# Performance work log

Measured on AMD Instinct MI355X. Metric: run time of the kernel, lower is better.

## Reference

```python
import jax, jax.numpy as jnp
import numpy as np

C = 256
CQK = C // 8


def setup_inputs() -> dict:
    key = jax.random.key(0)
    ks = jax.random.split(key, 8)
    B, H, W = 4, 64, 64
    x = jax.random.normal(ks[0], (B, C, H, W), dtype=jnp.float32)
    # 1x1 conv weights are plain [out_c, in_c] matrices + bias
    sq = 1.0 / np.sqrt(C)
    Wq = jax.random.uniform(ks[1], (CQK, C), jnp.float32, -sq, sq)
    bq = jax.random.uniform(ks[2], (CQK,), jnp.float32, -sq, sq)
    Wk = jax.random.uniform(ks[3], (CQK, C), jnp.float32, -sq, sq)
    bk = jax.random.uniform(ks[4], (CQK,), jnp.float32, -sq, sq)
    Wv = jax.random.uniform(ks[5], (C, C), jnp.float32, -sq, sq)
    bv = jax.random.uniform(ks[6], (C,), jnp.float32, -sq, sq)
    gamma = jnp.zeros((1,), dtype=jnp.float32)
    return {"x": x, "Wq": Wq, "bq": bq, "Wk": Wk, "bk": bk, "Wv": Wv, "bv": bv, "gamma": gamma}


def reference(x, Wq, bq, Wk, bk, Wv, bv, gamma):
    B, Cc, H, W = x.shape
    N = H * W
    xf = x.reshape(B, Cc, N)  # [B, C, N]
    # 1x1 convs == channel GEMMs
    q = jnp.einsum('dc,bcn->bdn', Wq, xf) + bq[None, :, None]  # [B, C/8, N]
    k = jnp.einsum('dc,bcn->bdn', Wk, xf) + bk[None, :, None]  # [B, C/8, N]
    v = jnp.einsum('dc,bcn->bdn', Wv, xf) + bv[None, :, None]  # [B, C, N]
    # attention[b, i, j] = softmax_j( q_i . k_j )  (no scaling, as in source)
    attn = jax.nn.softmax(jnp.einsum('bdn,bdm->bnm', q, k), axis=-1)  # [B, N, N]
    # out = value @ attention  (note: NOT attention^T, faithful to source)
    out = jnp.einsum('bcn,bnm->bcm', v, attn)  # [B, C, N]
    out = out.reshape(B, Cc, H, W)
    return gamma[0] * out + x
```

## Files before the change

### kernel.cpp

```cpp
#include <hip/hip_runtime.h>
#include <hip/hip_bf16.h>


#define NB 4
#define CC 256
#define NN 4096
#define L2E 1.44269504088896340f

typedef short  short4v  __attribute__((ext_vector_type(4)));
typedef short  short8v  __attribute__((ext_vector_type(8)));
typedef __bf16 bf16x8   __attribute__((ext_vector_type(8)));
typedef float  f32x4    __attribute__((ext_vector_type(4)));
typedef float  f32x16   __attribute__((ext_vector_type(16)));
typedef unsigned long u64x2 __attribute__((ext_vector_type(2)));
typedef unsigned int u32;
typedef unsigned long u64;

static __device__ __forceinline__ unsigned short f2bf(float f) {
  union { __bf16 h; unsigned short u; } v; v.h = (__bf16)f; return v.u;
}
static __device__ __forceinline__ float bf2f(unsigned short u) {
  union { unsigned u; float f; } v; v.u = (u32)u << 16; return v.f;
}

union FragU { short8v s; bf16x8 b; unsigned u[4]; };

static __device__ __forceinline__ bf16x8 ld_frag(const unsigned short* p) {
  FragU u; u.s = *(const short8v*)p; return u.b;
}

static __device__ __forceinline__ f32x16 zero16() {
  f32x16 v;
#pragma unroll
  for (int i = 0; i < 16; ++i) v[i] = 0.0f;
  return v;
}

static __device__ __forceinline__ f32x16 mfma32(bf16x8 a, bf16x8 b, f32x16 c) {
  return __builtin_amdgcn_mfma_f32_32x32x16_bf16(a, b, c, 0, 0, 0);
}
static __device__ __forceinline__ f32x16 mfma8(long a, long b, f32x16 c) {
  return __builtin_amdgcn_mfma_f32_32x32x16_fp8_fp8(a, b, c, 0, 0, 0);
}

__global__ __launch_bounds__(256) void k_wcvt(
    const float* __restrict__ Wq, const float* __restrict__ Wk,
    const float* __restrict__ Wv, unsigned short* __restrict__ Wb)
{
  const int i4 = blockIdx.x * 256 + threadIdx.x;
  const int e = i4 * 4;
  const int row = e >> 8, c = e & 255;
  const float* src = (row < 32) ? (Wq + row * 256 + c)
                   : (row < 64) ? (Wk + (row - 32) * 256 + c)
                                : (Wv + (row - 64) * 256 + c);
  f32x4 v = *(const f32x4*)src;
  short4v s;
#pragma unroll
  for (int j = 0; j < 4; ++j) s[j] = (short)f2bf(v[j]);
  *(short4v*)(Wb + e) = s;
}

__global__ __launch_bounds__(256) void k_proj(
    const float* __restrict__ x, const unsigned short* __restrict__ Wb,
    const float* __restrict__ bq, const float* __restrict__ bk,
    const float* __restrict__ bv,
    unsigned short* __restrict__ Qt, unsigned short* __restrict__ Kt,
    unsigned char* __restrict__ V8)
{
  __shared__ unsigned short xs[32][268];
  const int t = threadIdx.x;
  const int b = blockIdx.y;
  const int n0 = blockIdx.x * 32;
  const int w = t >> 6, l = t & 63, h = l >> 5, col = l & 31;

  const float* xb = x + (size_t)b * CC * NN;
  {
    const int c_off = t >> 3, nl = 4 * (t & 7);
#pragma unroll
    for (int c0 = 0; c0 < CC; c0 += 32) {
      int c = c0 + c_off;
      f32x4 v4 = *(const f32x4*)(xb + (size_t)c * NN + n0 + nl);
#pragma unroll
      for (int j = 0; j < 4; ++j) xs[nl + j][c] = f2bf(v4[j]);
    }
  }
  __syncthreads();

  for (int f = w; f < 10; f += 4) {
    const float* bsrc; int rowbase; int mode; int wrow;
    if (f == 0)      { bsrc = bq; rowbase = 0;            mode = 0; wrow = 0; }
    else if (f == 1) { bsrc = bk; rowbase = 0;            mode = 1; wrow = 32; }
    else             { bsrc = bv; rowbase = (f - 2) * 32; mode = 2; wrow = 64 + rowbase; }

    f32x16 acc0 = zero16();
    const unsigned short* wr = Wb + (size_t)(wrow + col) * 256 + 8 * h;

#pragma unroll
    for (int k0 = 0; k0 < CC; k0 += 16) {
      FragU a;
      a.s = *(const short8v*)(wr + k0);
      const unsigned short* p0 = &xs[col][k0 + 8 * h];
      FragU b0;
      short4v t0a = *(const short4v*)p0, t0b = *(const short4v*)(p0 + 4);
#pragma unroll
      for (int j = 0; j < 4; ++j) { b0.s[j] = t0a[j]; b0.s[4 + j] = t0b[j]; }
      acc0 = mfma32(a.b, b0.b, acc0);
    }

    const int n = n0 + col;
#pragma unroll
    for (int q = 0; q < 4; ++q) {
      f32x4 bias4 = *(const f32x4*)(bsrc + rowbase + 8 * q + 4 * h);
      float vals[4];
#pragma unroll
      for (int i = 0; i < 4; ++i) vals[i] = acc0[4 * q + i] + bias4[i];
      if (mode == 2) {
        const size_t tb = ((((size_t)b * 128 + (n >> 5)) * 2 + ((n >> 3) & 1)) * 256) * 16
                          + ((n >> 4) & 1) * 8 + (n & 7);
        u32 w01 = __builtin_amdgcn_cvt_pk_fp8_f32(vals[0], vals[1], 0, false);
        u32 w23 = __builtin_amdgcn_cvt_pk_fp8_f32(vals[2], vals[3], 0, false);
        const int cb0 = rowbase + 8 * q + 4 * h;
        V8[tb + (size_t)(cb0 + 0) * 16] = (unsigned char)(w01 & 0xff);
        V8[tb + (size_t)(cb0 + 1) * 16] = (unsigned char)((w01 >> 8) & 0xff);
        V8[tb + (size_t)(cb0 + 2) * 16] = (unsigned char)(w23 & 0xff);
        V8[tb + (size_t)(cb0 + 3) * 16] = (unsigned char)((w23 >> 8) & 0xff);
      } else {
        unsigned short* dst = (mode == 0) ? Qt : Kt;
        const float scale = (mode == 0) ? L2E : 1.0f;
        short4v s4;
#pragma unroll
        for (int i = 0; i < 4; ++i) s4[i] = (short)f2bf(vals[i] * scale);
        *(short4v*)(dst + ((size_t)b * NN + n) * 32 + 8 * q + 4 * h) = s4;
      }
    }
  }
}

__global__ __launch_bounds__(512) void k_rowstats(
    const unsigned short* __restrict__ Qt, const unsigned short* __restrict__ Kt,
    float* __restrict__ cbias)
{
  __shared__ float ssum[8][64];
  const int t = threadIdx.x;
  const int w = t >> 6, l = t & 63, h = l >> 5, col = l & 31;
  const int b = blockIdx.y;
  const int n0 = blockIdx.x * 64;
  const unsigned short* Qb = Qt + (size_t)b * NN * 32;
  const unsigned short* Kb = Kt + (size_t)b * NN * 32;

  bf16x8 bq00 = ld_frag(Qb + (size_t)(n0 + col) * 32 + 8 * h);
  bf16x8 bq01 = ld_frag(Qb + (size_t)(n0 + col) * 32 + 16 + 8 * h);
  bf16x8 bq10 = ld_frag(Qb + (size_t)(n0 + 32 + col) * 32 + 8 * h);
  bf16x8 bq11 = ld_frag(Qb + (size_t)(n0 + 32 + col) * 32 + 16 + 8 * h);

  float acc0 = 0.0f, acc1 = 0.0f;
  const int mbase = w * (NN / 8);
#pragma unroll 2
  for (int mt = 0; mt < 16; ++mt) {
    const int m0 = mbase + mt * 32;
    bf16x8 ak0 = ld_frag(Kb + (size_t)(m0 + col) * 32 + 8 * h);
    bf16x8 ak1 = ld_frag(Kb + (size_t)(m0 + col) * 32 + 16 + 8 * h);
    f32x16 S0 = zero16(), S1 = zero16();
    S0 = mfma32(ak0, bq00, S0);
    S0 = mfma32(ak1, bq01, S0);
    S1 = mfma32(ak0, bq10, S1);
    S1 = mfma32(ak1, bq11, S1);
    float p0 = 0.0f, p1 = 0.0f, p2 = 0.0f, p3 = 0.0f;
#pragma unroll
    for (int r = 0; r < 8; ++r) {
      p0 += __builtin_amdgcn_exp2f(S0[r]);
      p1 += __builtin_amdgcn_exp2f(S0[8 + r]);
      p2 += __builtin_amdgcn_exp2f(S1[r]);
      p3 += __builtin_amdgcn_exp2f(S1[8 + r]);
    }
    acc0 += p0 + p1;
    acc1 += p2 + p3;
  }
  acc0 += __shfl_xor(acc0, 32);
  acc1 += __shfl_xor(acc1, 32);

  if (l < 32) { ssum[w][l] = acc0; ssum[w][32 + l] = acc1; }
  __syncthreads();

  if (t < 64) {
    float s = 0.0f;
#pragma unroll
    for (int wv = 0; wv < 8; ++wv) s += ssum[wv][t];
    cbias[(size_t)b * NN + n0 + t] = -__builtin_amdgcn_logf(s);
  }
}

__global__ __launch_bounds__(512) void k_emat(
    const unsigned short* __restrict__ Qt, const unsigned short* __restrict__ Kt,
    const float* __restrict__ cbias, unsigned char* __restrict__ E8)
{
  const int t = threadIdx.x;
  const int w = t >> 6, l = t & 63, h = l >> 5, col = l & 31;
  const int b = blockIdx.y;
  const int n0 = blockIdx.x * 32;
  const unsigned short* Qb = Qt + (size_t)b * NN * 32;
  const unsigned short* Kb = Kt + (size_t)b * NN * 32;

  bf16x8 aq0 = ld_frag(Qb + (size_t)(n0 + col) * 32 + 8 * h);
  bf16x8 aq1 = ld_frag(Qb + (size_t)(n0 + col) * 32 + 16 + 8 * h);

  f32x4 cb4[4];
  const float* cbi = cbias + (size_t)b * NN + n0;
#pragma unroll
  for (int q = 0; q < 4; ++q) cb4[q] = *(const f32x4*)(cbi + 8 * q + 4 * h);

  const size_t gh_off = (size_t)(n0 >> 5) * 1024 + (size_t)h * 512 + (size_t)col * 16;

#pragma unroll 2
  for (int mt = 0; mt < 16; ++mt) {
    const int m0 = w * 512 + mt * 32;
    bf16x8 bk0 = ld_frag(Kb + (size_t)(m0 + col) * 32 + 8 * h);
    bf16x8 bk1 = ld_frag(Kb + (size_t)(m0 + col) * 32 + 16 + 8 * h);
    f32x16 S = zero16();
    S = mfma32(aq0, bk0, S);
    S = mfma32(aq1, bk1, S);

    float e[16];
#pragma unroll
    for (int q = 0; q < 4; ++q)
#pragma unroll
      for (int i = 0; i < 4; ++i)
        e[4 * q + i] = __builtin_amdgcn_exp2f(S[4 * q + i] + cb4[q][i]);

    u32 wA = __builtin_amdgcn_cvt_pk_fp8_f32(e[0], e[1], 0, false);
    wA = __builtin_amdgcn_cvt_pk_fp8_f32(e[2], e[3], wA, true);
    u32 wB = __builtin_amdgcn_cvt_pk_fp8_f32(e[4], e[5], 0, false);
    wB = __builtin_amdgcn_cvt_pk_fp8_f32(e[6], e[7], wB, true);
    u32 wC = __builtin_amdgcn_cvt_pk_fp8_f32(e[8], e[9], 0, false);
    wC = __builtin_amdgcn_cvt_pk_fp8_f32(e[10], e[11], wC, true);
    u32 wD = __builtin_amdgcn_cvt_pk_fp8_f32(e[12], e[13], 0, false);
    wD = __builtin_amdgcn_cvt_pk_fp8_f32(e[14], e[15], wD, true);
    asm("v_permlane32_swap_b32 %0, %1" : "+v"(wA), "+v"(wB));
    asm("v_permlane32_swap_b32 %0, %1" : "+v"(wC), "+v"(wD));
    u64x2 ev;
    ev[0] = ((u64)wB << 32) | wA;
    ev[1] = ((u64)wD << 32) | wC;

    unsigned char* st = E8 + ((size_t)b * 128 + (size_t)(w * 16 + mt)) * 131072 + gh_off;
    *(u64x2*)st = ev;
  }
}

__global__ __launch_bounds__(256) void k_pv(
    const unsigned char* __restrict__ E8, const unsigned char* __restrict__ V8,
    const float* __restrict__ x, const float* __restrict__ gamma,
    float* __restrict__ out)
{
  __shared__ unsigned short ldb[32][264];
  const int t = threadIdx.x;
  const int w = t >> 6, l = t & 63, h = l >> 5, col = l & 31;
  const int b = blockIdx.y;
  const int m0 = blockIdx.x * 32;
  const int cc = w * 64;

  const unsigned char* ep = E8 + ((size_t)b * 128 + blockIdx.x) * 131072
                            + (size_t)h * 512 + (size_t)col * 16;
  const unsigned char* vp = V8 + ((size_t)b * 256 + h) * 4096
                            + (size_t)(cc + col) * 16;

  f32x16 acc[2];
  acc[0] = zero16();
  acc[1] = zero16();

  u64x2 ePf[8], vAp[8], vBp[8];
#pragma unroll
  for (int s = 0; s < 8; ++s) {
    ePf[s] = *(const u64x2*)(ep + (size_t)s * 1024);
    vAp[s] = *(const u64x2*)(vp + (size_t)s * 8192);
    vBp[s] = *(const u64x2*)(vp + (size_t)s * 8192 + 512);
  }

  for (int gg = 0; gg < 128; gg += 8) {
#pragma unroll
    for (int s = 0; s < 8; ++s) {
      const int gn = gg + 8 + s;
      u64x2 nE = *(const u64x2*)(ep + (size_t)gn * 1024);
      u64x2 nvA = *(const u64x2*)(vp + (size_t)gn * 8192);
      u64x2 nvB = *(const u64x2*)(vp + (size_t)gn * 8192 + 512);
      acc[0] = mfma8((long)ePf[s][0], (long)vAp[s][0], acc[0]);
      acc[1] = mfma8((long)ePf[s][0], (long)vBp[s][0], acc[1]);
      acc[0] = mfma8((long)ePf[s][1], (long)vAp[s][1], acc[0]);
      acc[1] = mfma8((long)ePf[s][1], (long)vBp[s][1], acc[1]);
      ePf[s] = nE; vAp[s] = nvA; vBp[s] = nvB;
    }
  }

#pragma unroll
  for (int cf = 0; cf < 2; ++cf)
#pragma unroll
    for (int r = 0; r < 16; ++r) {
      int mloc = (r & 3) + 8 * (r >> 2) + 4 * h;
      ldb[mloc][cc + 32 * cf + col] = f2bf(acc[cf][r]);
    }
  __syncthreads();

  const float g = gamma[0];
  const int ci = t >> 3;
  const int m4 = (t & 7) * 4;
#pragma unroll
  for (int rnd = 0; rnd < 8; ++rnd) {
    const int c = 32 * rnd + ci;
    const size_t idx = ((size_t)b * CC + c) * NN + m0 + m4;
    f32x4 xv = *(const f32x4*)(x + idx);
    f32x4 o;
#pragma unroll
    for (int k = 0; k < 4; ++k) o[k] = g * bf2f(ldb[m4 + k][c]) + xv[k];
    *(f32x4*)(out + idx) = o;
  }
}

extern "C" void kernel_launch(void* const* d_in, const int* in_sizes, int n_in,
                              void* d_out, int out_size, void* d_ws, size_t ws_size,
                              hipStream_t stream) {
  const float* x     = (const float*)d_in[0];
  const float* Wq    = (const float*)d_in[1];
  const float* bq    = (const float*)d_in[2];
  const float* Wk    = (const float*)d_in[3];
  const float* bk    = (const float*)d_in[4];
  const float* Wv    = (const float*)d_in[5];
  const float* bv    = (const float*)d_in[6];
  const float* gamma = (const float*)d_in[7];
  float* out = (float*)d_out;

  char* ws = (char*)d_ws;
  unsigned short* Qt = (unsigned short*)(ws);
  unsigned short* Kt = (unsigned short*)(ws + (1u << 20));
  unsigned char*  V8 = (unsigned char*)(ws + (2u << 20));
  unsigned short* Wb = (unsigned short*)(ws + (6u << 20));
  float* cbias = (float*)(ws + (6u << 20) + (1u << 18));
  unsigned char* E8  = (unsigned char*)(ws + (7u << 20));

  k_wcvt<<<dim3(80), 256, 0, stream>>>(Wq, Wk, Wv, Wb);
  k_proj<<<dim3(NN / 32, NB), 256, 0, stream>>>(x, Wb, bq, bk, bv, Qt, Kt, V8);
  k_rowstats<<<dim3(NN / 64, NB), 512, 0, stream>>>(Qt, Kt, cbias);
  k_emat<<<dim3(NN / 32, NB), 512, 0, stream>>>(Qt, Kt, cbias, E8);
  k_pv<<<dim3(NN / 32, NB), 256, 0, stream>>>(E8, V8, x, gamma, out);
}
```

Measured before the change: 88.55 us.

## Stage E tiles through triple-buffered LDS with direct global-to-LDS loads in k_pv

Result: slower. 94.34 us (+6.5%).

```diff
diff --git a/kernel.cpp b/kernel.cpp
--- a/kernel.cpp
+++ b/kernel.cpp
@@ -15,6 +15,13 @@
 typedef unsigned long u64x2 __attribute__((ext_vector_type(2)));
 typedef unsigned int u32;
 typedef unsigned long u64;
+
+#define AS1 __attribute__((address_space(1)))
+#define AS3 __attribute__((address_space(3)))
+
+static __device__ __forceinline__ void gload16(const void* g, void* l) {
+  __builtin_amdgcn_global_load_lds((const AS1 u32*)g, (AS3 u32*)l, 16, 0, 0);
+}
 
 static __device__ __forceinline__ unsigned short f2bf(float f) {
   union { __bf16 h; unsigned short u; } v; v.h = (__bf16)f; return v.u;
@@ -246,11 +253,23 @@
   }
 }
 
+#define ESTAGE(G)                                                              \
+  {                                                                            \
+    const int bufg_ = (G) % 3;                                                 \
+    _Pragma("unroll")                                                          \
+    for (int s_ = 0; s_ < 4; ++s_) {                                           \
+      const int tile_ = (G) * 16 + w * 4 + s_;                                 \
+      gload16(ep + (size_t)tile_ * 1024 + (size_t)l * 16,                      \
+              &ebuf[bufg_][w * 4 + s_][0]);                                    \
+    }                                                                          \
+  }
+
 __global__ __launch_bounds__(256) void k_pv(
     const unsigned char* __restrict__ E8, const unsigned char* __restrict__ V8,
     const float* __restrict__ x, const float* __restrict__ gamma,
     float* __restrict__ out)
 {
+  __shared__ __align__(16) char ebuf[3][16][1024];
   __shared__ unsigned short ldb[32][264];
   const int t = threadIdx.x;
   const int w = t >> 6, l = t & 63, h = l >> 5, col = l & 31;
@@ -258,8 +277,7 @@
   const int m0 = blockIdx.x * 32;
   const int cc = w * 64;
 
-  const unsigned char* ep = E8 + ((size_t)b * 128 + blockIdx.x) * 131072
-                            + (size_t)h * 512 + (size_t)col * 16;
+  const unsigned char* ep = E8 + ((size_t)b * 128 + blockIdx.x) * 131072;
   const unsigned char* vp = V8 + ((size_t)b * 256 + h) * 4096
                             + (size_t)(cc + col) * 16;
 
@@ -267,27 +285,45 @@
   acc[0] = zero16();
   acc[1] = zero16();
 
-  u64x2 ePf[8], vAp[8], vBp[8];
+  ESTAGE(0)
+  ESTAGE(1)
+  u64x2 vAp[8], vBp[8];
 #pragma unroll
   for (int s = 0; s < 8; ++s) {
-    ePf[s] = *(const u64x2*)(ep + (size_t)s * 1024);
     vAp[s] = *(const u64x2*)(vp + (size_t)s * 8192);
     vBp[s] = *(const u64x2*)(vp + (size_t)s * 8192 + 512);
   }
-
-  for (int gg = 0; gg < 128; gg += 8) {
-#pragma unroll
-    for (int s = 0; s < 8; ++s) {
-      const int gn = gg + 8 + s;
-      u64x2 nE = *(const u64x2*)(ep + (size_t)gn * 1024);
-      u64x2 nvA = *(const u64x2*)(vp + (size_t)gn * 8192);
-      u64x2 nvB = *(const u64x2*)(vp + (size_t)gn * 8192 + 512);
-      acc[0] = mfma8((long)ePf[s][0], (long)vAp[s][0], acc[0]);
-      acc[1] = mfma8((long)ePf[s][0], (long)vBp[s][0], acc[1]);
-      acc[0] = mfma8((long)ePf[s][1], (long)vAp[s][1], acc[0]);
-      acc[1] = mfma8((long)ePf[s][1], (long)vBp[s][1], acc[1]);
-      ePf[s] = nE; vAp[s] = nvA; vBp[s] = nvB;
-    }
+  __builtin_amdgcn_sched_barrier(0);
+  asm volatile("s_waitcnt vmcnt(4)\n\ts_barrier" ::: "memory");
+  __builtin_amdgcn_sched_barrier(0);
+
+  for (int grp = 0; grp < 8; ++grp) {
+    if (grp + 2 < 8) ESTAGE(grp + 2)
+
+    const char* eb = &ebuf[grp % 3][0][(size_t)h * 512 + (size_t)col * 16];
+#pragma unroll
+    for (int sub = 0; sub < 2; ++sub) {
+#pragma unroll
+      for (int s = 0; s < 8; ++s) {
+        const int it = sub * 8 + s;
+        const int gn = grp * 16 + it + 8;
+        u64x2 E = *(const u64x2*)(eb + (size_t)it * 1024);
+        u64x2 nvA = *(const u64x2*)(vp + (size_t)gn * 8192);
+        u64x2 nvB = *(const u64x2*)(vp + (size_t)gn * 8192 + 512);
+        acc[0] = mfma8((long)E[0], (long)vAp[s][0], acc[0]);
+        acc[1] = mfma8((long)E[0], (long)vBp[s][0], acc[1]);
+        acc[0] = mfma8((long)E[1], (long)vAp[s][1], acc[0]);
+        acc[1] = mfma8((long)E[1], (long)vBp[s][1], acc[1]);
+        vAp[s] = nvA; vBp[s] = nvB;
+      }
+    }
+
+    __builtin_amdgcn_sched_barrier(0);
+    if (grp + 2 < 8)
+      asm volatile("s_waitcnt vmcnt(4) lgkmcnt(0)\n\ts_barrier" ::: "memory");
+    else
+      asm volatile("s_waitcnt vmcnt(0) lgkmcnt(0)\n\ts_barrier" ::: "memory");
+    __builtin_amdgcn_sched_barrier(0);
   }
 
 #pragma unroll
```

## Split k_pv channel work across 8 waves instead of 4

Applied to the files above, without the earlier changes.

Result: slower. 96.75 us (+9.3%).

```diff
diff --git a/kernel.cpp b/kernel.cpp
--- a/kernel.cpp
+++ b/kernel.cpp
@@ -246,7 +246,7 @@
   }
 }
 
-__global__ __launch_bounds__(256) void k_pv(
+__global__ __launch_bounds__(512) void k_pv(
     const unsigned char* __restrict__ E8, const unsigned char* __restrict__ V8,
     const float* __restrict__ x, const float* __restrict__ gamma,
     float* __restrict__ out)
@@ -256,23 +256,20 @@
   const int w = t >> 6, l = t & 63, h = l >> 5, col = l & 31;
   const int b = blockIdx.y;
   const int m0 = blockIdx.x * 32;
-  const int cc = w * 64;
+  const int cc = w * 32;
 
   const unsigned char* ep = E8 + ((size_t)b * 128 + blockIdx.x) * 131072
                             + (size_t)h * 512 + (size_t)col * 16;
   const unsigned char* vp = V8 + ((size_t)b * 256 + h) * 4096
                             + (size_t)(cc + col) * 16;
 
-  f32x16 acc[2];
-  acc[0] = zero16();
-  acc[1] = zero16();
-
-  u64x2 ePf[8], vAp[8], vBp[8];
+  f32x16 acc = zero16();
+
+  u64x2 ePf[8], vAp[8];
 #pragma unroll
   for (int s = 0; s < 8; ++s) {
     ePf[s] = *(const u64x2*)(ep + (size_t)s * 1024);
     vAp[s] = *(const u64x2*)(vp + (size_t)s * 8192);
-    vBp[s] = *(const u64x2*)(vp + (size_t)s * 8192 + 512);
   }
 
   for (int gg = 0; gg < 128; gg += 8) {
@@ -281,35 +278,30 @@
       const int gn = gg + 8 + s;
       u64x2 nE = *(const u64x2*)(ep + (size_t)gn * 1024);
       u64x2 nvA = *(const u64x2*)(vp + (size_t)gn * 8192);
-      u64x2 nvB = *(const u64x2*)(vp + (size_t)gn * 8192 + 512);
-      acc[0] = mfma8((long)ePf[s][0], (long)vAp[s][0], acc[0]);
-      acc[1] = mfma8((long)ePf[s][0], (long)vBp[s][0], acc[1]);
-      acc[0] = mfma8((long)ePf[s][1], (long)vAp[s][1], acc[0]);
-      acc[1] = mfma8((long)ePf[s][1], (long)vBp[s][1], acc[1]);
-      ePf[s] = nE; vAp[s] = nvA; vBp[s] = nvB;
-    }
-  }
-
-#pragma unroll
-  for (int cf = 0; cf < 2; ++cf)
-#pragma unroll
-    for (int r = 0; r < 16; ++r) {
-      int mloc = (r & 3) + 8 * (r >> 2) + 4 * h;
-      ldb[mloc][cc + 32 * cf + col] = f2bf(acc[cf][r]);
-    }
+      acc = mfma8((long)ePf[s][0], (long)vAp[s][0], acc);
+      acc = mfma8((long)ePf[s][1], (long)vAp[s][1], acc);
+      ePf[s] = nE; vAp[s] = nvA;
+    }
+  }
+
+#pragma unroll
+  for (int r = 0; r < 16; ++r) {
+    int mloc = (r & 3) + 8 * (r >> 2) + 4 * h;
+    ldb[mloc][cc + col] = f2bf(acc[r]);
+  }
   __syncthreads();
 
   const float g = gamma[0];
-  const int ci = t >> 3;
-  const int m4 = (t & 7) * 4;
-#pragma unroll
-  for (int rnd = 0; rnd < 8; ++rnd) {
-    const int c = 32 * rnd + ci;
-    const size_t idx = ((size_t)b * CC + c) * NN + m0 + m4;
+  const int ci = t >> 1;
+  const int mh = (t & 1) * 16;
+  const size_t base = ((size_t)b * CC + ci) * NN + m0 + mh;
+#pragma unroll
+  for (int k4 = 0; k4 < 4; ++k4) {
+    const size_t idx = base + 4 * k4;
     f32x4 xv = *(const f32x4*)(x + idx);
     f32x4 o;
 #pragma unroll
-    for (int k = 0; k < 4; ++k) o[k] = g * bf2f(ldb[m4 + k][c]) + xv[k];
+    for (int k = 0; k < 4; ++k) o[k] = g * bf2f(ldb[mh + 4 * k4 + k][ci]) + xv[k];
     *(f32x4*)(out + idx) = o;
   }
 }
@@ -339,5 +331,5 @@
   k_proj<<<dim3(NN / 32, NB), 256, 0, stream>>>(x, Wb, bq, bk, bv, Qt, Kt, V8);
   k_rowstats<<<dim3(NN / 64, NB), 512, 0, stream>>>(Qt, Kt, cbias);
   k_emat<<<dim3(NN / 32, NB), 512, 0, stream>>>(Qt, Kt, cbias, E8);
-  k_pv<<<dim3(NN / 32, NB), 256, 0, stream>>>(E8, V8, x, gamma, out);
-}
+  k_pv<<<dim3(NN / 32, NB), 512, 0, stream>>>(E8, V8, x, gamma, out);
+}
```
